# Kernel tuning notes

Measured on AMD Instinct MI355X. Metric: run time of the kernel, lower is better.

The kernel has to match this reference:

```python
import jax, jax.numpy as jnp
import numpy as np

LEAK_RATE = 0.95


def setup_inputs() -> dict:
    key = jax.random.key(0)
    k1, k2, k3, k4 = jax.random.split(key, 4)
    B, S, I, H = 32, 2048, 512, 1024
    x = jax.random.normal(k1, (B, S, I), dtype=jnp.float32)
    # W_in: kaiming-uniform-like input projection (frozen)
    bound = 1.0 / np.sqrt(I)
    W_in = jax.random.uniform(k2, (H, I), dtype=jnp.float32, minval=-bound, maxval=bound)
    # W_res: sparse random matrix rescaled to spectral radius 1.2 (frozen)
    W = jax.random.normal(k3, (H, H), dtype=jnp.float32)
    mask = (jax.random.uniform(k4, (H, H)) > 0.1).astype(jnp.float32)  # sparsity=0.1
    W = W * mask
    eig = np.linalg.eigvals(np.asarray(W))
    radius = np.max(np.abs(eig)).astype(np.float32)
    W_res = W * (1.2 / (radius + 1e-8))
    return {"x": x, "W_in": W_in, "W_res": W_res}


def reference(x, W_in, W_res):
    # x: [B, S, I]; W_in: [H, I]; W_res: [H, H]
    B = x.shape[0]
    H = W_res.shape[0]
    # Precompute input projection for all timesteps (batched GEMM)
    u = jnp.einsum('bsi,hi->bsh', x, W_in)  # [B, S, H]
    init = jnp.zeros((B, H), dtype=x.dtype)

    def step(prev, u_t):
        new = jnp.tanh(u_t + prev @ W_res.T)
        new = LEAK_RATE * new + (1.0 - LEAK_RATE) * prev
        return new, new

    _, states = jax.lax.scan(step, init, jnp.swapaxes(u, 0, 1))  # [S, B, H]
    return jnp.swapaxes(states, 0, 1)  # [B, S, H]
```

## Files before the change

kernel.cpp:

```cpp
#include <hip/hip_runtime.h>
#include <cmath>

#define LEAK 0.95f
#define ILEAK 0.05f

typedef float f4 __attribute__((ext_vector_type(4)));
typedef short s8 __attribute__((ext_vector_type(8)));
typedef unsigned long long ull;

__global__ __launch_bounds__(256) void resv_gemm_uin(
    const float* __restrict__ A, const float* __restrict__ Bm,
    float* __restrict__ C, int M, int N, int K)
{
    __shared__ float As[16][68];
    __shared__ float Bs[16][68];
    const int tid = threadIdx.x;
    const int m0 = blockIdx.y * 64;
    const int n0 = blockIdx.x * 64;
    const int lm = tid >> 2;
    const int lk = (tid & 3) * 4;
    const int ty = tid >> 4;
    const int tx = tid & 15;

    float acc[4][4];
#pragma unroll
    for (int i = 0; i < 4; ++i)
#pragma unroll
        for (int j = 0; j < 4; ++j) acc[i][j] = 0.f;

    const float* Aptr = A + (size_t)(m0 + lm) * K + lk;
    const float* Bptr = Bm + (size_t)(n0 + lm) * K + lk;

    for (int k0 = 0; k0 < K; k0 += 16) {
        float4 av = *(const float4*)(Aptr + k0);
        float4 bv = *(const float4*)(Bptr + k0);
        __syncthreads();
        As[lk + 0][lm] = av.x; As[lk + 1][lm] = av.y;
        As[lk + 2][lm] = av.z; As[lk + 3][lm] = av.w;
        Bs[lk + 0][lm] = bv.x; Bs[lk + 1][lm] = bv.y;
        Bs[lk + 2][lm] = bv.z; Bs[lk + 3][lm] = bv.w;
        __syncthreads();
#pragma unroll
        for (int kk = 0; kk < 16; ++kk) {
            float4 a = *(const float4*)(&As[kk][ty * 4]);
            float4 b = *(const float4*)(&Bs[kk][tx * 4]);
            acc[0][0] += a.x * b.x; acc[0][1] += a.x * b.y; acc[0][2] += a.x * b.z; acc[0][3] += a.x * b.w;
            acc[1][0] += a.y * b.x; acc[1][1] += a.y * b.y; acc[1][2] += a.y * b.z; acc[1][3] += a.y * b.w;
            acc[2][0] += a.z * b.x; acc[2][1] += a.z * b.y; acc[2][2] += a.z * b.z; acc[2][3] += a.z * b.w;
            acc[3][0] += a.w * b.x; acc[3][1] += a.w * b.y; acc[3][2] += a.w * b.z; acc[3][3] += a.w * b.w;
        }
    }
    float* Cp = C + (size_t)(m0 + ty * 4) * N + n0 + tx * 4;
#pragma unroll
    for (int i = 0; i < 4; ++i) {
        float4 v = make_float4(acc[i][0], acc[i][1], acc[i][2], acc[i][3]);
        *(float4*)(Cp + (size_t)i * N) = v;
    }
}

__device__ __forceinline__ ushort f32_to_bf16_rne(float x) {
    unsigned u = __float_as_uint(x);
    return (ushort)((u + 0x7FFFu + ((u >> 16) & 1u)) >> 16);
}

__global__ __launch_bounds__(256, 1) void resv_recur(
    const float* __restrict__ Wres,
    float* __restrict__ out,
    ull* __restrict__ pairs)
{
    constexpr int H = 1024, S = 2048;
    extern __shared__ char smraw[];
    ushort* Bq  = (ushort*)smraw;
    float*  uL  = (float*)(smraw + 8704);
    float*  red = (float*)(smraw + 8704 + 16384);

    const int tid = threadIdx.x;
    const int g  = blockIdx.x & 7;
    const int r  = blockIdx.x >> 3;
    const int h0 = r * 32;
    const int b0 = g * 4;

    const int w  = tid >> 6;
    const int l  = tid & 63;
    const int lg = l >> 4;
    const int lc = l & 15;

    s8 Afrag[16];
#pragma unroll
    for (int m = 0; m < 2; ++m)
#pragma unroll
        for (int kt = 0; kt < 8; ++kt) {
            const float* wp = Wres + (size_t)(h0 + m * 16 + lc) * H
                            + (w * 256 + kt * 32 + lg * 8);
            s8 a;
#pragma unroll
            for (int j = 0; j < 8; ++j) a[j] = (short)f32_to_bf16_rne(wp[j]);
            Afrag[m * 8 + kt] = a;
        }

    const int fb  = tid & 3;
    const int frw = tid >> 2;
    float pv = 0.f;

    ushort* BqW   = Bq + (size_t)w * 4 * 272;
    ushort* BqWr  = BqW + (l & 3) * 272 + (l >> 2);
    const ushort* bbase = BqW + (size_t)(lc & 3) * 272 + lg * 8;

    for (int t = 0; t < S; ++t) {
        if ((t & 15) == 0) {
            float* uB = uL + ((t >> 4) & 1) * 2048;
            for (int c = tid; c < 512; c += 256) {
                int rw4 = c & 7, b = (c >> 3) & 3, tt = c >> 5;
                const float4* src =
                    (const float4*)(out + ((size_t)(b0 + b) * S + (t + tt)) * H + h0);
                ((float4*)uB)[(tt * 4 + b) * 8 + rw4] = src[rw4];
            }
        }
        {
            const ull* src = pairs + ((size_t)((t & 1) * 8 + g)) * 4096
                           + (size_t)w * 1024 + l;
            const unsigned tgt = (unsigned)t;
            ull v[16];
            for (;;) {
#pragma unroll
                for (int c = 0; c < 16; ++c)
                    v[c] = __hip_atomic_load(src + c * 64, __ATOMIC_RELAXED,
                                             __HIP_MEMORY_SCOPE_AGENT);
                int ok = 1;
#pragma unroll
                for (int c = 0; c < 16; ++c)
                    ok &= ((unsigned)(v[c] >> 32) == tgt);
                if (__all(ok)) break;
            }
#pragma unroll
            for (int c = 0; c < 16; ++c)
                BqWr[c * 16] = f32_to_bf16_rne(__uint_as_float((unsigned)v[c]));
        }
        asm volatile("s_waitcnt lgkmcnt(0)" ::: "memory");
        __builtin_amdgcn_sched_barrier(0);

        f4 c0 = (f4)(0.f), c1 = (f4)(0.f);
#pragma unroll
        for (int kt = 0; kt < 8; ++kt) {
            s8 bf = *(const s8*)(bbase + kt * 32);
            c0 = __builtin_amdgcn_mfma_f32_16x16x32_bf16(Afrag[kt],     bf, c0, 0, 0, 0);
            c1 = __builtin_amdgcn_mfma_f32_16x16x32_bf16(Afrag[8 + kt], bf, c1, 0, 0, 0);
        }
        if (lc < 4) {
#pragma unroll
            for (int j = 0; j < 4; ++j) {
                red[(w * 32 + lg * 4 + j) * 4 + lc]      = c0[j];
                red[(w * 32 + 16 + lg * 4 + j) * 4 + lc] = c1[j];
            }
        }
        __syncthreads();

        if (tid < 128) {
            float sum = red[(0 * 32 + frw) * 4 + fb] + red[(1 * 32 + frw) * 4 + fb]
                      + red[(2 * 32 + frw) * 4 + fb] + red[(3 * 32 + frw) * 4 + fb];
            float uv = uL[((t >> 4) & 1) * 2048 + (((t & 15) * 4 + fb) << 5) + frw];
            float ns = LEAK * tanhf(uv + sum) + ILEAK * pv;
            pv = ns;
            ull pk = ((ull)(unsigned)(t + 1) << 32) |
                     (ull)__float_as_uint(ns);
            __hip_atomic_store(
                pairs + ((size_t)(((t + 1) & 1) * 8 + g)) * 4096 + h0 * 4 + tid,
                pk, __ATOMIC_RELAXED, __HIP_MEMORY_SCOPE_AGENT);
            out[((size_t)(b0 + fb) * S + t) * H + h0 + frw] = ns;
        }
        __syncthreads();
    }
}

extern "C" void kernel_launch(void* const* d_in, const int* in_sizes, int n_in,
                              void* d_out, int out_size, void* d_ws, size_t ws_size,
                              hipStream_t stream)
{
    const float* x    = (const float*)d_in[0];
    const float* Win  = (const float*)d_in[1];
    const float* Wres = (const float*)d_in[2];
    float* out = (float*)d_out;

    ull* pairs = (ull*)d_ws;

    hipMemsetAsync(d_ws, 0, 524288, stream);

    dim3 gemm_grid(1024 / 64, 65536 / 64);
    resv_gemm_uin<<<gemm_grid, 256, 0, stream>>>(x, Win, out, 65536, 1024, 512);

    constexpr int kLds = 96 * 1024;
    hipFuncSetAttribute((const void*)resv_recur,
                        hipFuncAttributeMaxDynamicSharedMemorySize, kLds);
    resv_recur<<<dim3(256), dim3(256), kLds, stream>>>(Wres, out, pairs);
}
```

Before: 5.192 ms.

## Replace FP32 SIMT input-projection GEMM with split-bf16 MFMA GEMM

Replaces the scalar FP32 tiled GEMM that computes the input projection with a matrix-core kernel. Each FP32 operand is split into a high and a low bf16 part, and three bf16 MFMAs (hi*hi, hi*lo, lo*hi) approximate FP32 accuracy. W_in tiles are converted and staged in LDS while x is read directly from global memory. This cuts the cost of the large GEMM ahead of the sequential recurrence, at the price of extra conversion work, 80KB of LDS per block (one block per CU), and slightly different rounding.

```diff
diff --git a/kernel.cpp b/kernel.cpp
--- a/kernel.cpp
+++ b/kernel.cpp
@@ -8,59 +8,97 @@
 typedef short s8 __attribute__((ext_vector_type(8)));
 typedef unsigned long long ull;
 
-__global__ __launch_bounds__(256) void resv_gemm_uin(
-    const float* __restrict__ A, const float* __restrict__ Bm,
-    float* __restrict__ C, int M, int N, int K)
-{
-    __shared__ float As[16][68];
-    __shared__ float Bs[16][68];
-    const int tid = threadIdx.x;
-    const int m0 = blockIdx.y * 64;
-    const int n0 = blockIdx.x * 64;
-    const int lm = tid >> 2;
-    const int lk = (tid & 3) * 4;
-    const int ty = tid >> 4;
-    const int tx = tid & 15;
-
-    float acc[4][4];
-#pragma unroll
-    for (int i = 0; i < 4; ++i)
-#pragma unroll
-        for (int j = 0; j < 4; ++j) acc[i][j] = 0.f;
-
-    const float* Aptr = A + (size_t)(m0 + lm) * K + lk;
-    const float* Bptr = Bm + (size_t)(n0 + lm) * K + lk;
-
-    for (int k0 = 0; k0 < K; k0 += 16) {
-        float4 av = *(const float4*)(Aptr + k0);
-        float4 bv = *(const float4*)(Bptr + k0);
-        __syncthreads();
-        As[lk + 0][lm] = av.x; As[lk + 1][lm] = av.y;
-        As[lk + 2][lm] = av.z; As[lk + 3][lm] = av.w;
-        Bs[lk + 0][lm] = bv.x; Bs[lk + 1][lm] = bv.y;
-        Bs[lk + 2][lm] = bv.z; Bs[lk + 3][lm] = bv.w;
-        __syncthreads();
-#pragma unroll
-        for (int kk = 0; kk < 16; ++kk) {
-            float4 a = *(const float4*)(&As[kk][ty * 4]);
-            float4 b = *(const float4*)(&Bs[kk][tx * 4]);
-            acc[0][0] += a.x * b.x; acc[0][1] += a.x * b.y; acc[0][2] += a.x * b.z; acc[0][3] += a.x * b.w;
-            acc[1][0] += a.y * b.x; acc[1][1] += a.y * b.y; acc[1][2] += a.y * b.z; acc[1][3] += a.y * b.w;
-            acc[2][0] += a.z * b.x; acc[2][1] += a.z * b.y; acc[2][2] += a.z * b.z; acc[2][3] += a.z * b.w;
-            acc[3][0] += a.w * b.x; acc[3][1] += a.w * b.y; acc[3][2] += a.w * b.z; acc[3][3] += a.w * b.w;
-        }
-    }
-    float* Cp = C + (size_t)(m0 + ty * 4) * N + n0 + tx * 4;
-#pragma unroll
-    for (int i = 0; i < 4; ++i) {
-        float4 v = make_float4(acc[i][0], acc[i][1], acc[i][2], acc[i][3]);
-        *(float4*)(Cp + (size_t)i * N) = v;
-    }
-}
-
 __device__ __forceinline__ ushort f32_to_bf16_rne(float x) {
     unsigned u = __float_as_uint(x);
     return (ushort)((u + 0x7FFFu + ((u >> 16) & 1u)) >> 16);
+}
+__device__ __forceinline__ float bf16_to_f32(ushort h) {
+    return __uint_as_float(((unsigned)h) << 16);
+}
+
+__global__ __launch_bounds__(256, 1) void resv_gemm_mfma(
+    const float* __restrict__ A,
+    const float* __restrict__ Bm,
+    float* __restrict__ C)
+{
+    constexpr int K = 512;
+    extern __shared__ char sm[];
+    ushort* Bh = (ushort*)sm;
+    ushort* Bl = (ushort*)(sm + 40960);
+
+    const int tid = threadIdx.x;
+    const int n0 = blockIdx.x * 128;
+    const int m0 = blockIdx.y * 64;
+    const int w  = tid >> 6;
+    const int l  = tid & 63;
+    const int lg = l >> 4;
+    const int lc = l & 15;
+
+    f4 acc[8];
+#pragma unroll
+    for (int i = 0; i < 8; ++i) acc[i] = (f4)(0.f);
+
+    const int scol = tid >> 1;
+    const int skh  = (tid & 1) * 64;
+    const int sntk = scol >> 4;
+    const int slc  = scol & 15;
+
+    const float* aprow = A + (size_t)(m0 + 16 * w + lc) * K + lg * 8;
+
+    for (int kc = 0; kc < 4; ++kc) {
+        __syncthreads();
+        {
+            const float* bp = Bm + (size_t)(n0 + scol) * K + kc * 128 + skh;
+#pragma unroll
+            for (int i = 0; i < 16; ++i) {
+                float4 v = *(const float4*)(bp + 4 * i);
+                int k  = skh + 4 * i;
+                int kt = k >> 5, kk = k & 31;
+                ushort h0 = f32_to_bf16_rne(v.x);
+                ushort h1 = f32_to_bf16_rne(v.y);
+                ushort h2 = f32_to_bf16_rne(v.z);
+                ushort h3 = f32_to_bf16_rne(v.w);
+                ushort q0 = f32_to_bf16_rne(v.x - bf16_to_f32(h0));
+                ushort q1 = f32_to_bf16_rne(v.y - bf16_to_f32(h1));
+                ushort q2 = f32_to_bf16_rne(v.z - bf16_to_f32(h2));
+                ushort q3 = f32_to_bf16_rne(v.w - bf16_to_f32(h3));
+                int off = (sntk * 4 + kt) * 640 + slc * 40 + kk;
+                *(ull*)(Bh + off) = (ull)h0 | ((ull)h1 << 16)
+                                  | ((ull)h2 << 32) | ((ull)h3 << 48);
+                *(ull*)(Bl + off) = (ull)q0 | ((ull)q1 << 16)
+                                  | ((ull)q2 << 32) | ((ull)q3 << 48);
+            }
+        }
+        __syncthreads();
+#pragma unroll
+        for (int kt = 0; kt < 4; ++kt) {
+            float4 a0 = *(const float4*)(aprow + kc * 128 + kt * 32);
+            float4 a1 = *(const float4*)(aprow + kc * 128 + kt * 32 + 4);
+            float av[8] = {a0.x, a0.y, a0.z, a0.w, a1.x, a1.y, a1.z, a1.w};
+            s8 ah, al;
+#pragma unroll
+            for (int j = 0; j < 8; ++j) {
+                ushort h = f32_to_bf16_rne(av[j]);
+                ah[j] = (short)h;
+                al[j] = (short)f32_to_bf16_rne(av[j] - bf16_to_f32(h));
+            }
+#pragma unroll
+            for (int nt = 0; nt < 8; ++nt) {
+                const int boff = (nt * 4 + kt) * 640 + lc * 40 + lg * 8;
+                s8 bh = *(const s8*)(Bh + boff);
+                s8 bl = *(const s8*)(Bl + boff);
+                acc[nt] = __builtin_amdgcn_mfma_f32_16x16x32_bf16(ah, bh, acc[nt], 0, 0, 0);
+                acc[nt] = __builtin_amdgcn_mfma_f32_16x16x32_bf16(ah, bl, acc[nt], 0, 0, 0);
+                acc[nt] = __builtin_amdgcn_mfma_f32_16x16x32_bf16(al, bh, acc[nt], 0, 0, 0);
+            }
+        }
+    }
+#pragma unroll
+    for (int nt = 0; nt < 8; ++nt)
+#pragma unroll
+        for (int j = 0; j < 4; ++j)
+            C[(size_t)(m0 + 16 * w + 4 * lg + j) * 1024 + n0 + nt * 16 + lc] =
+                acc[nt][j];
 }
 
 __global__ __launch_bounds__(256, 1) void resv_recur(
@@ -185,8 +223,10 @@
 
     hipMemsetAsync(d_ws, 0, 524288, stream);
 
-    dim3 gemm_grid(1024 / 64, 65536 / 64);
-    resv_gemm_uin<<<gemm_grid, 256, 0, stream>>>(x, Win, out, 65536, 1024, 512);
+    constexpr int kGemmLds = 81920;
+    hipFuncSetAttribute((const void*)resv_gemm_mfma,
+                        hipFuncAttributeMaxDynamicSharedMemorySize, kGemmLds);
+    resv_gemm_mfma<<<dim3(8, 1024), 256, kGemmLds, stream>>>(x, Win, out);
 
     constexpr int kLds = 96 * 1024;
     hipFuncSetAttribute((const void*)resv_recur,
```

After: 4.842 ms. 6.7% less time.
